# Kernel tuning notes

Measured on AMD Instinct MI355X. Metric: run time of the kernel, lower is better.

Reference implementation:

```python
import jax, jax.numpy as jnp
import numpy as np

M, N = 4096, 4096

def _make_expk(n):
    k = np.arange(n, dtype=np.float64) * np.pi / (2.0 * n)
    return jnp.asarray(np.stack([np.cos(k), np.sin(k)], axis=-1), dtype=jnp.float32)

def setup_inputs() -> dict:
    key = jax.random.key(0)
    x = jax.random.normal(key, (M, N), dtype=jnp.float32)
    return {"x": x, "expkM": _make_expk(M), "expkN": _make_expk(N)}

def _idct_last(X, expk):
    """1D IDCT (inverse of unnormalized DCT-II) along last axis via Makhoul's
    N-point FFT trick. expk[k] = (cos, sin) of pi*k/(2N), i.e. e^{j pi k/(2N)}."""
    n = X.shape[-1]
    Xv = X * 0.5
    # V[k] = (Xv[k] - j*Xv[n-k]) * e^{j pi k/(2n)}, with imag part 0 at k=0
    tail = -jnp.flip(Xv, axis=-1)[..., :-1]
    Vi = jnp.concatenate([jnp.zeros_like(Xv[..., :1]), tail], axis=-1)
    W = expk[:, 0] + 1j * expk[:, 1]
    V = (Xv + 1j * Vi) * W
    v = jnp.fft.ifft(V, axis=-1).real.astype(X.dtype)
    # de-interleave: out[2m] = v[m], out[2m+1] = v[n-1-m]
    out = jnp.zeros_like(X)
    out = out.at[..., 0::2].set(v[..., : n - n // 2])
    out = out.at[..., 1::2].set(jnp.flip(v, axis=-1)[..., : n // 2])
    return out

def reference(x, expkM, expkN):
    # separable 2D IDCT: last axis (N) then first axis (M)
    y = _idct_last(x, expkN)
    y = _idct_last(y.T, expkM).T
    return y
```

## Files before the change

### kernel.cpp

```cpp
#include <hip/hip_runtime.h>
#include <math.h>


#define TT 256

constexpr float W64R[32] = {
    1.0f, 0.995184726672197f, 0.980785280403230f, 0.956940335732209f,
    0.923879532511287f, 0.881921264348355f, 0.831469612302545f, 0.773010453362737f,
    0.707106781186548f, 0.634393284163645f, 0.555570233019602f, 0.471396736825998f,
    0.382683432365090f, 0.290284677254462f, 0.195090322016128f, 0.0980171403295606f,
    0.0f, -0.0980171403295606f, -0.195090322016128f, -0.290284677254462f,
    -0.382683432365090f, -0.471396736825998f, -0.555570233019602f, -0.634393284163645f,
    -0.707106781186548f, -0.773010453362737f, -0.831469612302545f, -0.881921264348355f,
    -0.923879532511287f, -0.956940335732209f, -0.980785280403230f, -0.995184726672197f};
constexpr float W64I[32] = {
    0.0f, 0.0980171403295606f, 0.195090322016128f, 0.290284677254462f,
    0.382683432365090f, 0.471396736825998f, 0.555570233019602f, 0.634393284163645f,
    0.707106781186548f, 0.773010453362737f, 0.831469612302545f, 0.881921264348355f,
    0.923879532511287f, 0.956940335732209f, 0.980785280403230f, 0.995184726672197f,
    1.0f, 0.995184726672197f, 0.980785280403230f, 0.956940335732209f,
    0.923879532511287f, 0.881921264348355f, 0.831469612302545f, 0.773010453362737f,
    0.707106781186548f, 0.634393284163645f, 0.555570233019602f, 0.471396736825998f,
    0.382683432365090f, 0.290284677254462f, 0.195090322016128f, 0.0980171403295606f};

__device__ __forceinline__ constexpr int brev(int x, int bits) {
    int r = 0;
    for (int i = 0; i < bits; ++i) { r = (r << 1) | (x & 1); x >>= 1; }
    return r;
}

__device__ __forceinline__ float vadd(float a, float b) { return a + b; }
__device__ __forceinline__ float vsub(float a, float b) { return a - b; }
__device__ __forceinline__ float vmul(float a, float s) { return a * s; }
__device__ __forceinline__ float2 vadd(float2 a, float2 b) { return make_float2(a.x + b.x, a.y + b.y); }
__device__ __forceinline__ float2 vsub(float2 a, float2 b) { return make_float2(a.x - b.x, a.y - b.y); }
__device__ __forceinline__ float2 vmul(float2 a, float s) { return make_float2(a.x * s, a.y * s); }

template <int NP, typename V>
__device__ __forceinline__ void fft_dif(V* re, V* im) {
#pragma unroll
    for (int h = NP / 2; h >= 1; h >>= 1) {
#pragma unroll
        for (int b = 0; b < NP; b += 2 * h) {
#pragma unroll
            for (int k = 0; k < h; ++k) {
                V ur = re[b + k], ui = im[b + k];
                V vr = re[b + k + h], vi = im[b + k + h];
                V dr = vsub(ur, vr), di = vsub(ui, vi);
                re[b + k] = vadd(ur, vr);
                im[b + k] = vadd(ui, vi);
                float wr = W64R[k * (32 / h)], wi = W64I[k * (32 / h)];
                re[b + k + h] = vsub(vmul(dr, wr), vmul(di, wi));
                im[b + k + h] = vadd(vmul(dr, wi), vmul(di, wr));
            }
        }
    }
}

__global__ void tw_init_kernel(float2* __restrict__ tw2048,
                               float2* __restrict__ ca, float2* __restrict__ cb,
                               float2* __restrict__ cc, float2* __restrict__ cd) {
    int k = blockIdx.x * TT + threadIdx.x;
    const double s = 0.5 / 4096.0;
    double aw = M_PI * (double)k / 2048.0;
    double wr = cos(aw), wi = sin(aw);
    double a1 = M_PI * (double)k / 8192.0;
    double e1r = cos(a1), e1i = sin(a1);
    double a2 = M_PI * (double)(k + 2048) / 8192.0;
    double e2r = cos(a2), e2i = sin(a2);
    double Ar = s * ((1.0 - wi) * e1r - wr * e1i);
    double Ai = s * ((1.0 - wi) * e1i + wr * e1r);
    double Br = (k == 0) ? 0.0 : Ai;
    double Bi = (k == 0) ? 0.0 : -Ar;
    double Cr = s * ((1.0 + wi) * e2r + wr * e2i);
    double Ci = s * ((1.0 + wi) * e2i - wr * e2r);
    ca[k] = make_float2((float)Ar, (float)Ai);
    cb[k] = make_float2((float)Br, (float)Bi);
    cc[k] = make_float2((float)Cr, (float)Ci);
    cd[k] = make_float2((float)Ci, (float)-Cr);
    double at = M_PI * (double)k / 1024.0;
    tw2048[k] = make_float2((float)cos(at), (float)sin(at));
}

__global__ __launch_bounds__(TT) void col_a_kernel(
    const float* __restrict__ x,
    const float2* __restrict__ ca, const float2* __restrict__ cb,
    const float2* __restrict__ cc, const float2* __restrict__ cd,
    const float2* __restrict__ tw2048, float2* __restrict__ T1) {
    int c2 = blockIdx.x * 64 + threadIdx.x;
    int k1 = blockIdx.y * 4 + threadIdx.y;
    const float2* __restrict__ xv = (const float2*)x;
    float2 fr[32], fi[32];
#pragma unroll
    for (int k2 = 0; k2 < 32; ++k2) {
        int k = k1 + 64 * k2;
        float2 xa = xv[(size_t)k * 2048 + c2];
        float2 xb = xv[(size_t)((4096 - k) & 4095) * 2048 + c2];
        float2 xc = xv[(size_t)(2048 + k) * 2048 + c2];
        float2 xd = xv[(size_t)(2048 - k) * 2048 + c2];
        float2 A = ca[k], B = cb[k], C = cc[k], D = cd[k];
        fr[k2] = make_float2(A.x * xa.x + B.x * xb.x + C.x * xc.x + D.x * xd.x,
                             A.x * xa.y + B.x * xb.y + C.x * xc.y + D.x * xd.y);
        fi[k2] = make_float2(A.y * xa.x + B.y * xb.x + C.y * xc.x + D.y * xd.x,
                             A.y * xa.y + B.y * xb.y + C.y * xc.y + D.y * xd.y);
    }
    fft_dif<32, float2>(fr, fi);
#pragma unroll
    for (int j = 0; j < 32; ++j) {
        int n2 = brev(j, 5);
        float2 w = tw2048[k1 * n2];
        float2 orr = vsub(vmul(fr[j], w.x), vmul(fi[j], w.y));
        float2 oii = vadd(vmul(fr[j], w.y), vmul(fi[j], w.x));
        float4 o = make_float4(orr.x, oii.x, orr.y, oii.y);
        *(float4*)&T1[(size_t)(k1 * 32 + n2) * 4096 + 2 * c2] = o;
    }
}

__global__ __launch_bounds__(TT) void col_b_kernel(
    const float2* __restrict__ T1, float* __restrict__ out) {
    __shared__ float L[128 * 68];
    int tx = threadIdx.x, ty = threadIdx.y;
    int c = blockIdx.x * 64 + tx;
    int n2 = blockIdx.y * 4 + ty;
    float re[64], im[64];
#pragma unroll
    for (int k1 = 0; k1 < 64; ++k1) {
        float2 v = T1[(size_t)(k1 * 32 + n2) * 4096 + c];
        re[k1] = v.x; im[k1] = v.y;
    }
    fft_dif<64, float>(re, im);
    int tlin = ty * 64 + tx;
#pragma unroll
    for (int g = 0; g < 4; ++g) {
        if (ty == g) {
#pragma unroll
            for (int j = 0; j < 64; ++j) {
                int n1 = brev(j, 6);
                L[(2 * n1) * 68 + tx] = re[j];
                L[(2 * n1 + 1) * 68 + tx] = im[j];
            }
        }
        __syncthreads();
        int n2g = blockIdx.y * 4 + g;
#pragma unroll
        for (int u = 0; u < 8; ++u) {
            int idx = tlin + 256 * u;
            int slot = idx >> 4, xp = idx & 15;
            int n1 = slot >> 1;
            int m = 32 * n1 + n2g;
            int row = (n1 < 32) ? (4 * m + ((slot & 1) ? 2 : 0))
                                : (((slot & 1) ? 8189 : 8191) - 4 * m);
            float4 v = *(const float4*)&L[slot * 68 + 4 * xp];
            *(float4*)&out[(size_t)row * 4096 + blockIdx.x * 64 + 4 * xp] = v;
        }
        __syncthreads();
    }
}

#define C_SQ2 0.70710678118654752440f
__device__ __forceinline__ void radix8(const float* ar, const float* ai,
                                       float* tr, float* ti) {
    float s04r = ar[0] + ar[4], s04i = ai[0] + ai[4];
    float d04r = ar[0] - ar[4], d04i = ai[0] - ai[4];
    float s26r = ar[2] + ar[6], s26i = ai[2] + ai[6];
    float d26r = ar[2] - ar[6], d26i = ai[2] - ai[6];
    float E0r = s04r + s26r, E0i = s04i + s26i;
    float E1r = d04r - d26i, E1i = d04i + d26r;
    float E2r = s04r - s26r, E2i = s04i - s26i;
    float E3r = d04r + d26i, E3i = d04i - d26r;
    float s15r = ar[1] + ar[5], s15i = ai[1] + ai[5];
    float d15r = ar[1] - ar[5], d15i = ai[1] - ai[5];
    float s37r = ar[3] + ar[7], s37i = ai[3] + ai[7];
    float d37r = ar[3] - ar[7], d37i = ai[3] - ai[7];
    float O0r = s15r + s37r, O0i = s15i + s37i;
    float O1r = d15r - d37i, O1i = d15i + d37r;
    float O2r = s15r - s37r, O2i = s15i - s37i;
    float O3r = d15r + d37i, O3i = d15i - d37r;
    float W1r = C_SQ2 * (O1r - O1i), W1i = C_SQ2 * (O1r + O1i);
    float W2r = -O2i, W2i = O2r;
    float W3r = -C_SQ2 * (O3r + O3i), W3i = C_SQ2 * (O3r - O3i);
    tr[0] = E0r + O0r; ti[0] = E0i + O0i;
    tr[4] = E0r - O0r; ti[4] = E0i - O0i;
    tr[1] = E1r + W1r; ti[1] = E1i + W1i;
    tr[5] = E1r - W1r; ti[5] = E1i - W1i;
    tr[2] = E2r + W2r; ti[2] = E2i + W2i;
    tr[6] = E2r - W2r; ti[6] = E2i - W2i;
    tr[3] = E3r + W3r; ti[3] = E3i + W3i;
    tr[7] = E3r - W3r; ti[7] = E3i - W3i;
}

__global__ __launch_bounds__(TT) void idct_rows_kernel(
    const float2* __restrict__ ca, const float2* __restrict__ cb,
    const float2* __restrict__ cc, const float2* __restrict__ cd,
    const float2* __restrict__ tw2048, float* __restrict__ io) {
    __shared__ float pool[8576];
    float* b0r = pool;
    float* b0i = pool + 2112;
    float* b1r = pool + 4224;
    float* b1i = pool + 6400;
    float* stg = pool + 4224;
    const int t = threadIdx.x;
    float* __restrict__ xr = io + (size_t)blockIdx.x * 4096;

#pragma unroll
    for (int u = 0; u < 4; ++u) {
        int idx = t + 256 * u;
        float4 v = ((const float4*)xr)[idx];
        *(float4*)&stg[4 * idx] = v;
    }
    __syncthreads();

    float zr[8], zi[8], tr[8], ti[8];
#pragma unroll
    for (int p = 0; p < 8; ++p) {
        int k = t + 256 * p;
        float xa = stg[k];
        float xb = stg[(4096 - k) & 4095];
        float xc = stg[2048 + k];
        float xd = stg[2048 - k];
        float2 A = ca[k], B = cb[k], C = cc[k], D = cd[k];
        zr[p] = A.x * xa + B.x * xb + C.x * xc + D.x * xd;
        zi[p] = A.y * xa + B.y * xb + C.y * xc + D.y * xd;
    }
    radix8(zr, zi, tr, ti);
    {
        int baseA = 8 * t + (t >> 2);
        b0r[baseA] = tr[0]; b0i[baseA] = ti[0];
#pragma unroll
        for (int q = 1; q < 8; ++q) {
            float2 w = tw2048[(t * q) & 2047];
            b0r[baseA + q] = w.x * tr[q] - w.y * ti[q];
            b0i[baseA + q] = w.x * ti[q] + w.y * tr[q];
        }
    }
    __syncthreads();
    {
        float ar[8], ai[8];
        int rb = t + (t >> 5);
#pragma unroll
        for (int p = 0; p < 8; ++p) { ar[p] = b0r[rb + 264 * p]; ai[p] = b0i[rb + 264 * p]; }
        radix8(ar, ai, tr, ti);
        int j = t >> 3, k = t & 7, wj = 8 * j;
        int baseB = 68 * j + k;
        b1r[baseB] = tr[0]; b1i[baseB] = ti[0];
#pragma unroll
        for (int q = 1; q < 8; ++q) {
            int off = baseB + 8 * q + (q >> 1);
            float2 w = tw2048[(wj * q) & 2047];
            b1r[off] = w.x * tr[q] - w.y * ti[q];
            b1i[off] = w.x * ti[q] + w.y * tr[q];
        }
    }
    __syncthreads();
    {
        float ar[8], ai[8];
        int rb = t + (t >> 4);
#pragma unroll
        for (int p = 0; p < 8; ++p) { ar[p] = b1r[rb + 272 * p]; ai[p] = b1i[rb + 272 * p]; }
        radix8(ar, ai, tr, ti);
        int j = t >> 6, wj = 64 * j, k = t & 63;
        int baseC = 528 * j + k + (k >> 5);
        b0r[baseC] = tr[0]; b0i[baseC] = ti[0];
#pragma unroll
        for (int q = 1; q < 8; ++q) {
            int off = baseC + 66 * q;
            float2 w = tw2048[(wj * q) & 2047];
            b0r[off] = w.x * tr[q] - w.y * ti[q];
            b0i[off] = w.x * ti[q] + w.y * tr[q];
        }
    }
    __syncthreads();
#pragma unroll
    for (int u = 0; u < 2; ++u) {
        int b = t + 256 * u;
        int rb = b + (b >> 5);
        int wb = b + (b >> 4);
        float a0r = b0r[rb], a0i = b0i[rb];
        float a1r = b0r[rb + 528], a1i = b0i[rb + 528];
        float a2r = b0r[rb + 1056], a2i = b0i[rb + 1056];
        float a3r = b0r[rb + 1584], a3i = b0i[rb + 1584];
        float s02r = a0r + a2r, s02i = a0i + a2i;
        float d02r = a0r - a2r, d02i = a0i - a2i;
        float s13r = a1r + a3r, s13i = a1i + a3i;
        float d13r = a1r - a3r, d13i = a1i - a3i;
        b1r[wb] = s02r + s13r;          b1i[wb] = s02i + s13i;
        b1r[wb + 544] = d02r - d13i;    b1i[wb + 544] = d02i + d13r;
        b1r[wb + 1088] = s02r - s13r;   b1i[wb + 1088] = s02i - s13i;
        b1r[wb + 1632] = d02r + d13i;   b1i[wb + 1632] = d02i - d13r;
    }
    __syncthreads();
#pragma unroll
    for (int i = 0; i < 4; ++i) {
        int s = t + 256 * i;
        int l2 = 2047 - s;
        int ms = s + (s >> 4);
        int ml = l2 + (l2 >> 4);
        float4 o = make_float4(b1r[ms], b1i[ml], b1i[ms], b1r[ml]);
        *(float4*)&xr[4 * s] = o;
    }
}

extern "C" void kernel_launch(void* const* d_in, const int* in_sizes, int n_in,
                              void* d_out, int out_size, void* d_ws, size_t ws_size,
                              hipStream_t stream) {
    const float* x = (const float*)d_in[0];
    float* out = (float*)d_out;

    float2* tw2048 = (float2*)d_ws;
    float2* ca = (float2*)((char*)d_ws + 1 * 16384);
    float2* cb = (float2*)((char*)d_ws + 2 * 16384);
    float2* cc = (float2*)((char*)d_ws + 3 * 16384);
    float2* cd = (float2*)((char*)d_ws + 4 * 16384);
    float2* T1 = (float2*)((char*)d_ws + (1 << 20));

    tw_init_kernel<<<8, TT, 0, stream>>>(tw2048, ca, cb, cc, cd);
    col_a_kernel<<<dim3(32, 16), dim3(64, 4), 0, stream>>>(x, ca, cb, cc, cd, tw2048, T1);
    col_b_kernel<<<dim3(64, 8), dim3(64, 4), 0, stream>>>(T1, out);
    idct_rows_kernel<<<4096, TT, 0, stream>>>(ca, cb, cc, cd, tw2048, out);
}
```

Measured before the change: 201.3 us.

## Shrink per-thread FFT state in column kernels to raise occupancy

col_a now handles one column per thread with scalar loads instead of two columns through float2, which halves the register arrays and doubles the grid. col_b splits each 64-point column FFT across two threads as even/odd 32-point FFTs and combines them with a radix-2 step through shared memory, using launch_bounds of 4 blocks per SM. The aim is fewer registers per thread, more waves in flight, and more blocks. In exchange, global loads and stores become narrower (scalar or float2 instead of float4), the output writes are no longer vectorized rows, and col_b gains extra shared-memory traffic and barrier rounds.

```diff
diff --git a/kernel.cpp b/kernel.cpp
--- a/kernel.cpp
+++ b/kernel.cpp
@@ -82,76 +82,85 @@
     tw2048[k] = make_float2((float)cos(at), (float)sin(at));
 }
 
-__global__ __launch_bounds__(TT) void col_a_kernel(
+__global__ __launch_bounds__(TT, 4) void col_a_kernel(
     const float* __restrict__ x,
     const float2* __restrict__ ca, const float2* __restrict__ cb,
     const float2* __restrict__ cc, const float2* __restrict__ cd,
     const float2* __restrict__ tw2048, float2* __restrict__ T1) {
-    int c2 = blockIdx.x * 64 + threadIdx.x;
+    int c = blockIdx.x * 64 + threadIdx.x;
     int k1 = blockIdx.y * 4 + threadIdx.y;
-    const float2* __restrict__ xv = (const float2*)x;
-    float2 fr[32], fi[32];
+    float fr[32], fi[32];
 #pragma unroll
     for (int k2 = 0; k2 < 32; ++k2) {
         int k = k1 + 64 * k2;
-        float2 xa = xv[(size_t)k * 2048 + c2];
-        float2 xb = xv[(size_t)((4096 - k) & 4095) * 2048 + c2];
-        float2 xc = xv[(size_t)(2048 + k) * 2048 + c2];
-        float2 xd = xv[(size_t)(2048 - k) * 2048 + c2];
+        float xa = x[(size_t)k * 4096 + c];
+        float xb = x[(size_t)((4096 - k) & 4095) * 4096 + c];
+        float xc = x[(size_t)(2048 + k) * 4096 + c];
+        float xd = x[(size_t)(2048 - k) * 4096 + c];
         float2 A = ca[k], B = cb[k], C = cc[k], D = cd[k];
-        fr[k2] = make_float2(A.x * xa.x + B.x * xb.x + C.x * xc.x + D.x * xd.x,
-                             A.x * xa.y + B.x * xb.y + C.x * xc.y + D.x * xd.y);
-        fi[k2] = make_float2(A.y * xa.x + B.y * xb.x + C.y * xc.x + D.y * xd.x,
-                             A.y * xa.y + B.y * xb.y + C.y * xc.y + D.y * xd.y);
-    }
-    fft_dif<32, float2>(fr, fi);
+        fr[k2] = A.x * xa + B.x * xb + C.x * xc + D.x * xd;
+        fi[k2] = A.y * xa + B.y * xb + C.y * xc + D.y * xd;
+    }
+    fft_dif<32, float>(fr, fi);
 #pragma unroll
     for (int j = 0; j < 32; ++j) {
         int n2 = brev(j, 5);
         float2 w = tw2048[k1 * n2];
-        float2 orr = vsub(vmul(fr[j], w.x), vmul(fi[j], w.y));
-        float2 oii = vadd(vmul(fr[j], w.y), vmul(fi[j], w.x));
-        float4 o = make_float4(orr.x, oii.x, orr.y, oii.y);
-        *(float4*)&T1[(size_t)(k1 * 32 + n2) * 4096 + 2 * c2] = o;
-    }
-}
-
-__global__ __launch_bounds__(TT) void col_b_kernel(
+        float2 o = make_float2(fr[j] * w.x - fi[j] * w.y,
+                               fr[j] * w.y + fi[j] * w.x);
+        T1[(size_t)(k1 * 32 + n2) * 4096 + c] = o;
+    }
+}
+
+__global__ __launch_bounds__(TT, 4) void col_b_kernel(
     const float2* __restrict__ T1, float* __restrict__ out) {
-    __shared__ float L[128 * 68];
-    int tx = threadIdx.x, ty = threadIdx.y;
+    __shared__ float2 EO[2][32][64];
+    int tx = threadIdx.x;
+    int ty = threadIdx.y;
+    int tz = ty & 1;
+    int g  = ty >> 1;
     int c = blockIdx.x * 64 + tx;
-    int n2 = blockIdx.y * 4 + ty;
-    float re[64], im[64];
-#pragma unroll
-    for (int k1 = 0; k1 < 64; ++k1) {
+    int n2 = blockIdx.y * 2 + g;
+    float fr[32], fi[32];
+#pragma unroll
+    for (int a = 0; a < 32; ++a) {
+        int k1 = 2 * a + tz;
         float2 v = T1[(size_t)(k1 * 32 + n2) * 4096 + c];
-        re[k1] = v.x; im[k1] = v.y;
-    }
-    fft_dif<64, float>(re, im);
-    int tlin = ty * 64 + tx;
-#pragma unroll
-    for (int g = 0; g < 4; ++g) {
-        if (ty == g) {
-#pragma unroll
-            for (int j = 0; j < 64; ++j) {
-                int n1 = brev(j, 6);
-                L[(2 * n1) * 68 + tx] = re[j];
-                L[(2 * n1 + 1) * 68 + tx] = im[j];
+        fr[a] = v.x; fi[a] = v.y;
+    }
+    fft_dif<32, float>(fr, fi);
+#pragma unroll
+    for (int gg = 0; gg < 2; ++gg) {
+        if (g == gg) {
+#pragma unroll
+            for (int j = 0; j < 32; ++j) {
+                int n = brev(j, 5);
+                float vr = fr[j], vi = fi[j];
+                if (tz) {
+                    float wr = W64R[n], wi = W64I[n];
+                    float t2 = vr * wr - vi * wi;
+                    vi = vr * wi + vi * wr;
+                    vr = t2;
+                }
+                EO[tz][n][tx] = make_float2(vr, vi);
             }
         }
         __syncthreads();
-        int n2g = blockIdx.y * 4 + g;
-#pragma unroll
-        for (int u = 0; u < 8; ++u) {
-            int idx = tlin + 256 * u;
-            int slot = idx >> 4, xp = idx & 15;
-            int n1 = slot >> 1;
-            int m = 32 * n1 + n2g;
-            int row = (n1 < 32) ? (4 * m + ((slot & 1) ? 2 : 0))
-                                : (((slot & 1) ? 8189 : 8191) - 4 * m);
-            float4 v = *(const float4*)&L[slot * 68 + 4 * xp];
-            *(float4*)&out[(size_t)row * 4096 + blockIdx.x * 64 + 4 * xp] = v;
+        if (g == gg) {
+#pragma unroll
+            for (int n = 0; n < 32; ++n) {
+                float2 E  = EO[0][n][tx];
+                float2 WO = EO[1][n][tx];
+                float zr, zi;
+                if (tz == 0) { zr = E.x + WO.x; zi = E.y + WO.y; }
+                else         { zr = E.x - WO.x; zi = E.y - WO.y; }
+                int n1 = tz * 32 + n;
+                int m = 32 * n1 + n2;
+                int r_re = (n1 < 32) ? 4 * m     : 8191 - 4 * m;
+                int r_im = (n1 < 32) ? 4 * m + 2 : 8189 - 4 * m;
+                out[(size_t)r_re * 4096 + c] = zr;
+                out[(size_t)r_im * 4096 + c] = zi;
+            }
         }
         __syncthreads();
     }
@@ -314,7 +323,7 @@
     float2* T1 = (float2*)((char*)d_ws + (1 << 20));
 
     tw_init_kernel<<<8, TT, 0, stream>>>(tw2048, ca, cb, cc, cd);
-    col_a_kernel<<<dim3(32, 16), dim3(64, 4), 0, stream>>>(x, ca, cb, cc, cd, tw2048, T1);
-    col_b_kernel<<<dim3(64, 8), dim3(64, 4), 0, stream>>>(T1, out);
+    col_a_kernel<<<dim3(64, 16), dim3(64, 4), 0, stream>>>(x, ca, cb, cc, cd, tw2048, T1);
+    col_b_kernel<<<dim3(64, 16), dim3(64, 4), 0, stream>>>(T1, out);
     idct_rows_kernel<<<4096, TT, 0, stream>>>(ca, cb, cc, cd, tw2048, out);
 }
```

Result: no change. 204.3 us (+1.5%).
